# Kernel tuning notes

Hardware: AMD Instinct MI355X
Metric: run time of the kernel (lower is better)

Reference implementation:

```python
import jax, jax.numpy as jnp
import numpy as np

B, D, E, C = 16384, 2048, 16, 64  # batch, feat_dim, num_experts, classes per expert
CLASS_STARTS = np.arange(E, dtype=np.int32) * C  # contiguous equal-size class ranges


def setup_inputs() -> dict:
    key = jax.random.key(0)
    k1, k2, k3, k4, k5 = jax.random.split(key, 5)
    return {
        "features": jax.random.normal(k1, (B, D), dtype=jnp.float32),
        "coarse_w": jax.random.normal(k2, (E, D), dtype=jnp.float32) * 0.02,
        "coarse_b": jax.random.normal(k3, (E,), dtype=jnp.float32) * 0.02,
        "expert_w": jax.random.normal(k4, (E, C, D), dtype=jnp.float32) * 0.02,
        "expert_b": jax.random.normal(k5, (E, C), dtype=jnp.float32) * 0.02,
    }


def reference(features, coarse_w, coarse_b, expert_w, expert_b):
    # coarse router: Linear(feat_dim -> num_experts)
    coarse_output = features @ coarse_w.T + coarse_b          # [B, E]
    expert_id = jnp.argmax(coarse_output, axis=1)             # [B] top-1 routing

    # all-expert heads as one batched GEMM, then select routed expert per sample
    # (same math as gather-by-mask + per-expert Linear + scatter-back loop)
    y_all = jnp.einsum('bd,ecd->bec', features, expert_w) + expert_b  # [B, E, C]
    y = jnp.take_along_axis(y_all, expert_id[:, None, None], axis=1)[:, 0, :]  # [B, C]

    # local_preds: softmax probs of the routed expert (all experts have C = max classes)
    local_preds = jax.nn.softmax(y, axis=1)                   # [B, C]

    # global prediction = local argmax + expert's class-range start
    starts = jnp.asarray(CLASS_STARTS)
    global_preds = (jnp.argmax(y, axis=1) + starts[expert_id]).astype(jnp.float32)  # [B]

    return coarse_output, expert_id, local_preds, global_preds
```

## Files before the change

### kernel.cpp

```cpp
#include <hip/hip_runtime.h>
#include <cstdint>

static constexpr int B_ = 16384;
static constexpr int D_ = 2048;
static constexpr int E_ = 16;
static constexpr int C_ = 64;
static constexpr int KCH = 32;
static constexpr int TR_E = 64;
static constexpr int SK_E = 4;
static constexpr int TR_C = 128;
static constexpr int SK_C = 8;
static constexpr int MAXITEMS = (B_ / TR_E) + E_;

template <int RPT, int CPT, int NC, int TR, int SK, bool FLAT>
__global__ __launch_bounds__(256) void gemm_tile(
    const float* __restrict__ feat, const float* __restrict__ Wall,
    const int* __restrict__ rowList, const int* __restrict__ cnt,
    const int* __restrict__ sched, const int* __restrict__ nItems,
    float* __restrict__ part0,
    float* __restrict__ partRest)
{
  constexpr int FITER = TR / 32;
  constexpr int WSLOTS = NC * 8;
  constexpr int WITER = (WSLOTS + 255) / 256;
  constexpr int CG = NC / CPT;

  __shared__ float fT[KCH * TR];
  __shared__ float wT[KCH * NC];
  __shared__ int rIdx[TR];

  const int tid = threadIdx.x;
  int e, tile, kz;
  if (FLAT) {
    const int b = blockIdx.x;
    kz = b % SK;
    const int item = b / SK;
    if (item >= *nItems) return;
    const int s = sched[item];
    e = s & 255;
    tile = s >> 8;
  } else {
    e = 0;
    tile = blockIdx.x;
    kz = blockIdx.z;
  }
  const int count = cnt ? cnt[e] : B_;

  if (tid < TR) {
    const int slot = tile * TR + tid;
    rIdx[tid] = (slot < count) ? (rowList ? rowList[e * B_ + slot] : slot) : 0;
  }
  __syncthreads();

  unsigned grows[FITER];
  int dcf[FITER], sbf[FITER];
#pragma unroll
  for (int i = 0; i < FITER; ++i) {
    const int idx = i * 256 + tid;
    const int rl = idx >> 3;
    dcf[i] = idx & 7;
    grows[i] = (unsigned)rIdx[rl];
    sbf[i] = (((rl >> 3) ^ dcf[i]) << 3) + (rl & 7);
  }
  int wc[WITER], wdc[WITER], wsb[WITER];
  bool wact[WITER];
#pragma unroll
  for (int i = 0; i < WITER; ++i) {
    const int idx = i * 256 + tid;
    wact[i] = idx < WSLOTS;
    const int c = (idx < WSLOTS) ? (idx >> 3) : 0;
    wc[i] = c;
    wdc[i] = idx & 7;
    wsb[i] = (((c >> 3) ^ (wdc[i] & (NC / 8 - 1))) << 3) + (c & 7);
  }

  const int cg = tid % CG;
  const int rg = tid / CG;

  float acc[RPT][CPT];
#pragma unroll
  for (int r = 0; r < RPT; ++r)
#pragma unroll
    for (int c = 0; c < CPT; ++c) acc[r][c] = 0.f;

  const float* We = Wall + (size_t)e * NC * D_;
  constexpr int KRANGE = D_ / SK;
  constexpr int NCH = KRANGE / KCH;
  const int k0 = kz * KRANGE;

  float4 pf[FITER], pw[WITER];
#pragma unroll
  for (int i = 0; i < FITER; ++i)
    pf[i] = *(const float4*)(feat + (size_t)grows[i] * D_ + k0 + dcf[i] * 4);
#pragma unroll
  for (int i = 0; i < WITER; ++i)
    if (wact[i])
      pw[i] = *(const float4*)(We + (size_t)wc[i] * D_ + k0 + wdc[i] * 4);

  for (int ch = 0; ch < NCH; ++ch) {
#pragma unroll
    for (int i = 0; i < FITER; ++i) {
      float* p = &fT[(dcf[i] * 4) * TR + sbf[i]];
      p[0 * TR] = pf[i].x;
      p[1 * TR] = pf[i].y;
      p[2 * TR] = pf[i].z;
      p[3 * TR] = pf[i].w;
    }
#pragma unroll
    for (int i = 0; i < WITER; ++i)
      if (wact[i]) {
        float* p = &wT[(wdc[i] * 4) * NC + wsb[i]];
        p[0 * NC] = pw[i].x;
        p[1 * NC] = pw[i].y;
        p[2 * NC] = pw[i].z;
        p[3 * NC] = pw[i].w;
      }
    __syncthreads();
    if (ch + 1 < NCH) {
      const int kb = k0 + (ch + 1) * KCH;
#pragma unroll
      for (int i = 0; i < FITER; ++i)
        pf[i] = *(const float4*)(feat + (size_t)grows[i] * D_ + kb + dcf[i] * 4);
#pragma unroll
      for (int i = 0; i < WITER; ++i)
        if (wact[i])
          pw[i] = *(const float4*)(We + (size_t)wc[i] * D_ + kb + wdc[i] * 4);
    }
#pragma unroll
    for (int dd = 0; dd < KCH; ++dd) {
      const int s = dd >> 2;
      const int sw = s & (NC / 8 - 1);
      float a[RPT], bb[CPT];
#pragma unroll
      for (int r4 = 0; r4 < RPT / 4; ++r4) {
        const int col = rg * RPT + r4 * 4;
        const float4 v =
            *(const float4*)&fT[dd * TR + (((col >> 3) ^ s) << 3) + (col & 7)];
        a[r4 * 4 + 0] = v.x;
        a[r4 * 4 + 1] = v.y;
        a[r4 * 4 + 2] = v.z;
        a[r4 * 4 + 3] = v.w;
      }
      if constexpr (CPT >= 4) {
#pragma unroll
        for (int c4 = 0; c4 < CPT / 4; ++c4) {
          const int col = cg * CPT + c4 * 4;
          const float4 v =
              *(const float4*)&wT[dd * NC + (((col >> 3) ^ sw) << 3) + (col & 7)];
          bb[c4 * 4 + 0] = v.x;
          bb[c4 * 4 + 1] = v.y;
          bb[c4 * 4 + 2] = v.z;
          bb[c4 * 4 + 3] = v.w;
        }
      } else {
        const int col = cg * 2;
        const float2 v =
            *(const float2*)&wT[dd * NC + (((col >> 3) ^ sw) << 3) + (col & 7)];
        bb[0] = v.x;
        bb[1] = v.y;
      }
#pragma unroll
      for (int r = 0; r < RPT; ++r)
#pragma unroll
        for (int c = 0; c < CPT; ++c) acc[r][c] += a[r] * bb[c];
    }
    __syncthreads();
  }

  float* pk = kz ? (partRest + (size_t)(kz - 1) * B_ * NC) : part0;
#pragma unroll
  for (int r = 0; r < RPT; ++r) {
    const int lrow = rg * RPT + r;
    const int slot = tile * TR + lrow;
    if (slot < count) {
      const int grow = rIdx[lrow];
      float* dst = pk + (size_t)grow * NC + cg * CPT;
      if constexpr (CPT >= 4) {
#pragma unroll
        for (int c4 = 0; c4 < CPT / 4; ++c4)
          *(float4*)(dst + c4 * 4) =
              make_float4(acc[r][c4 * 4 + 0], acc[r][c4 * 4 + 1],
                          acc[r][c4 * 4 + 2], acc[r][c4 * 4 + 3]);
      } else {
        *(float2*)dst = make_float2(acc[r][0], acc[r][1]);
      }
    }
  }
}

__global__ __launch_bounds__(256) void coarse_finish(
    const float* __restrict__ cpart0, const float* __restrict__ cpartRest,
    const float* __restrict__ cb, float* __restrict__ out0,
    float* __restrict__ out1, int* __restrict__ eidArr, int* __restrict__ cnt,
    int* __restrict__ rowList) {
  __shared__ int lcnt[E_];
  __shared__ int lbase[E_];
  const int tid = threadIdx.x;
  if (tid < E_) lcnt[tid] = 0;
  __syncthreads();
  const int row = blockIdx.x * 256 + tid;

  float v[E_];
#pragma unroll
  for (int j = 0; j < E_; ++j) v[j] = cb[j];
#pragma unroll
  for (int kz = 0; kz < SK_C; ++kz) {
    const float* p = (kz == 0) ? (cpart0 + (size_t)row * E_)
                               : (cpartRest + ((size_t)(kz - 1) * B_ + row) * E_);
#pragma unroll
    for (int j4 = 0; j4 < E_ / 4; ++j4) {
      const float4 t = *(const float4*)(p + j4 * 4);
      v[j4 * 4 + 0] += t.x;
      v[j4 * 4 + 1] += t.y;
      v[j4 * 4 + 2] += t.z;
      v[j4 * 4 + 3] += t.w;
    }
  }
  int best = 0;
  float bv = v[0];
#pragma unroll
  for (int j = 1; j < E_; ++j)
    if (v[j] > bv) { bv = v[j]; best = j; }

  float* o0 = out0 + (size_t)row * E_;
#pragma unroll
  for (int j4 = 0; j4 < E_ / 4; ++j4)
    *(float4*)(o0 + j4 * 4) = make_float4(v[j4 * 4 + 0], v[j4 * 4 + 1],
                                          v[j4 * 4 + 2], v[j4 * 4 + 3]);
  out1[row] = (float)best;
  eidArr[row] = best;

  const int lpos = atomicAdd(&lcnt[best], 1);
  __syncthreads();
  if (tid < E_) lbase[tid] = atomicAdd(&cnt[tid], lcnt[tid]);
  __syncthreads();
  rowList[best * B_ + lbase[best] + lpos] = row;
}

__global__ void make_schedule(const int* __restrict__ cnt,
                              int* __restrict__ sched,
                              int* __restrict__ nItems) {
  __shared__ int tiles[E_];
  __shared__ int offs[E_];
  const int t = threadIdx.x;
  if (t < E_) tiles[t] = (cnt[t] + TR_E - 1) / TR_E;
  __syncthreads();
  if (t == 0) {
    int acc = 0;
    for (int e = 0; e < E_; ++e) {
      offs[e] = acc;
      acc += tiles[e];
    }
    *nItems = acc;
  }
  __syncthreads();
  if (t < E_) {
    const int o = offs[t], n = tiles[t];
    for (int k = 0; k < n; ++k) sched[o + k] = t | (k << 8);
  }
}

__global__ __launch_bounds__(256) void finish_rows(
    const float* __restrict__ ypart0, const float* __restrict__ ypartRest,
    const float* __restrict__ eb, const int* __restrict__ eidArr,
    float* __restrict__ out2, float* __restrict__ out3) {
  const int lane = threadIdx.x & 63;
  const int row = (blockIdx.x * 256 + threadIdx.x) >> 6;
  const int eid = eidArr[row];

  float v = eb[eid * C_ + lane];
  v += ypart0[(size_t)row * C_ + lane];
#pragma unroll
  for (int kz = 1; kz < SK_E; ++kz)
    v += ypartRest[((size_t)(kz - 1) * B_ + row) * C_ + lane];

  float m = v;
#pragma unroll
  for (int off = 32; off; off >>= 1) m = fmaxf(m, __shfl_xor(m, off, 64));
  const float p = __expf(v - m);
  float s = p;
#pragma unroll
  for (int off = 32; off; off >>= 1) s += __shfl_xor(s, off, 64);
  out2[(size_t)row * C_ + lane] = p / s;

  float av = v;
  int ai = lane;
#pragma unroll
  for (int off = 32; off; off >>= 1) {
    const float ov = __shfl_xor(av, off, 64);
    const int oi = __shfl_xor(ai, off, 64);
    if (ov > av || (ov == av && oi < ai)) { av = ov; ai = oi; }
  }
  if (lane == 0) out3[row] = (float)(ai + (eid << 6));
}

extern "C" void kernel_launch(void* const* d_in, const int* in_sizes, int n_in,
                              void* d_out, int out_size, void* d_ws,
                              size_t ws_size, hipStream_t stream) {
  const float* feat = (const float*)d_in[0];
  const float* cw = (const float*)d_in[1];
  const float* cb = (const float*)d_in[2];
  const float* ew = (const float*)d_in[3];
  const float* eb = (const float*)d_in[4];

  float* out0 = (float*)d_out;
  float* out1 = out0 + (size_t)B_ * E_;
  float* out2 = out1 + B_;
  float* out3 = out2 + (size_t)B_ * C_;

  char* ws = (char*)d_ws;
  float* cpartRest = (float*)ws;
  float* ypartRest = cpartRest + (size_t)(SK_C - 1) * B_ * E_;
  int* rowList = (int*)(ypartRest + (size_t)(SK_E - 1) * B_ * C_);
  int* cnt = rowList + (size_t)E_ * B_;
  int* eidArr = cnt + 64;
  int* sched = eidArr + B_;
  int* nItems = sched + 512;

  hipMemsetAsync(cnt, 0, E_ * sizeof(int), stream);

  gemm_tile<4, 2, E_, TR_C, SK_C, false>
      <<<dim3(B_ / TR_C, 1, SK_C), 256, 0, stream>>>(
          feat, cw, nullptr, nullptr, nullptr, nullptr, out0, cpartRest);
  coarse_finish<<<B_ / 256, 256, 0, stream>>>(out0, cpartRest, cb, out0, out1,
                                              eidArr, cnt, rowList);
  make_schedule<<<1, 64, 0, stream>>>(cnt, sched, nItems);
  gemm_tile<4, 4, C_, TR_E, SK_E, true>
      <<<MAXITEMS * SK_E, 256, 0, stream>>>(feat, ew, rowList, cnt, sched,
                                            nItems, out2, ypartRest);
  finish_rows<<<(B_ * 64) / 256, 256, 0, stream>>>(out2, ypartRest, eb, eidArr,
                                                   out2, out3);
}
```

Before: 298.5 us.

## Pre-transpose weights, read weights from global via scalar loads, widen tiles

Adds a kernel that transposes the expert and coarse weights into a D-major layout, then redesigns the GEMM tile. Each wave now owns a slice of columns and reads its weights straight from global memory with wave-uniform addresses, while only the features are staged in padded shared memory, and the math uses packed two-wide FMAs. Tile rows are doubled, and split-K depth is doubled when the workspace is large enough. The goals are to remove the LDS traffic and swizzle work for weights and to add parallelism. The costs are an extra transpose pass over about 8 MB of weights on every call and more partial-sum traffic in the finish kernels.

```diff
diff --git a/kernel.cpp b/kernel.cpp
--- a/kernel.cpp
+++ b/kernel.cpp
@@ -1,32 +1,70 @@
 #include <hip/hip_runtime.h>
 #include <cstdint>
+
+typedef float v2f __attribute__((ext_vector_type(2)));
 
 static constexpr int B_ = 16384;
 static constexpr int D_ = 2048;
 static constexpr int E_ = 16;
 static constexpr int C_ = 64;
 static constexpr int KCH = 32;
-static constexpr int TR_E = 64;
-static constexpr int SK_E = 4;
-static constexpr int TR_C = 128;
-static constexpr int SK_C = 8;
+
+static constexpr int TR_E = 128;
+static constexpr int TR_C = 256;
+static constexpr int SK_E_HI = 8;
+static constexpr int SK_C_HI = 16;
+static constexpr int SK_E_LO = 4;
+static constexpr int SK_C_LO = 8;
 static constexpr int MAXITEMS = (B_ / TR_E) + E_;
 
-template <int RPT, int CPT, int NC, int TR, int SK, bool FLAT>
+__global__ __launch_bounds__(256) void transpose_w(
+    const float* __restrict__ ew, const float* __restrict__ cw,
+    float* __restrict__ ewT, float* __restrict__ cwT) {
+  const int bid = blockIdx.x;
+  const int tid = threadIdx.x;
+  if (bid < 128) {
+    const int g = bid * 256 + tid;
+    const int eidx = g >> 11;
+    const int d = g & (D_ - 1);
+    const float* src = ew + ((size_t)eidx * C_) * D_ + d;
+    float* dst = ewT + ((size_t)eidx * D_ + d) * C_;
+#pragma unroll
+    for (int cc = 0; cc < C_; cc += 16) {
+      float t[16];
+#pragma unroll
+      for (int c = 0; c < 16; ++c) t[c] = src[(size_t)(cc + c) * D_];
+#pragma unroll
+      for (int q = 0; q < 4; ++q)
+        *(float4*)(dst + cc + q * 4) =
+            make_float4(t[q * 4 + 0], t[q * 4 + 1], t[q * 4 + 2], t[q * 4 + 3]);
+    }
+  } else {
+    const int d = (bid - 128) * 256 + tid;
+    float t[E_];
+#pragma unroll
+    for (int e2 = 0; e2 < E_; ++e2) t[e2] = cw[(size_t)e2 * D_ + d];
+    float* dst = cwT + (size_t)d * E_;
+#pragma unroll
+    for (int q = 0; q < 4; ++q)
+      *(float4*)(dst + q * 4) =
+          make_float4(t[q * 4 + 0], t[q * 4 + 1], t[q * 4 + 2], t[q * 4 + 3]);
+  }
+}
+
+template <int RPT, int CW, int NC, int TR, int SK, bool FLAT>
 __global__ __launch_bounds__(256) void gemm_tile(
-    const float* __restrict__ feat, const float* __restrict__ Wall,
+    const float* __restrict__ feat, const float* __restrict__ Wt,
     const int* __restrict__ rowList, const int* __restrict__ cnt,
     const int* __restrict__ sched, const int* __restrict__ nItems,
     float* __restrict__ part0,
     float* __restrict__ partRest)
 {
+  constexpr int TRP = TR + 1;
   constexpr int FITER = TR / 32;
-  constexpr int WSLOTS = NC * 8;
-  constexpr int WITER = (WSLOTS + 255) / 256;
-  constexpr int CG = NC / CPT;
-
-  __shared__ float fT[KCH * TR];
-  __shared__ float wT[KCH * NC];
+  static_assert(64 * RPT == TR, "lanes*RPT must cover tile rows");
+  static_assert(4 * CW == NC, "4 waves * CW must cover tile cols");
+
+  __shared__ float fT[KCH * TRP];
   __shared__ int rIdx[TR];
 
   const int tid = threadIdx.x;
@@ -44,6 +82,9 @@
     tile = blockIdx.x;
     kz = blockIdx.z;
   }
+  e = __builtin_amdgcn_readfirstlane(e);
+  tile = __builtin_amdgcn_readfirstlane(tile);
+  kz = __builtin_amdgcn_readfirstlane(kz);
   const int count = cnt ? cnt[e] : B_;
 
   if (tid < TR) {
@@ -53,116 +94,67 @@
   __syncthreads();
 
   unsigned grows[FITER];
-  int dcf[FITER], sbf[FITER];
+  int dcf[FITER], rls[FITER];
 #pragma unroll
   for (int i = 0; i < FITER; ++i) {
     const int idx = i * 256 + tid;
-    const int rl = idx >> 3;
+    rls[i] = idx >> 3;
     dcf[i] = idx & 7;
-    grows[i] = (unsigned)rIdx[rl];
-    sbf[i] = (((rl >> 3) ^ dcf[i]) << 3) + (rl & 7);
-  }
-  int wc[WITER], wdc[WITER], wsb[WITER];
-  bool wact[WITER];
-#pragma unroll
-  for (int i = 0; i < WITER; ++i) {
-    const int idx = i * 256 + tid;
-    wact[i] = idx < WSLOTS;
-    const int c = (idx < WSLOTS) ? (idx >> 3) : 0;
-    wc[i] = c;
-    wdc[i] = idx & 7;
-    wsb[i] = (((c >> 3) ^ (wdc[i] & (NC / 8 - 1))) << 3) + (c & 7);
-  }
-
-  const int cg = tid % CG;
-  const int rg = tid / CG;
-
-  float acc[RPT][CPT];
+    grows[i] = (unsigned)rIdx[rls[i]];
+  }
+
+  const int lane = tid & 63;
+  const int w = __builtin_amdgcn_readfirstlane(tid >> 6);
+  const int wcol = w * CW;
+
+  v2f acc[RPT][CW / 2];
 #pragma unroll
   for (int r = 0; r < RPT; ++r)
 #pragma unroll
-    for (int c = 0; c < CPT; ++c) acc[r][c] = 0.f;
-
-  const float* We = Wall + (size_t)e * NC * D_;
+    for (int j = 0; j < CW / 2; ++j) acc[r][j] = (v2f){0.f, 0.f};
+
   constexpr int KRANGE = D_ / SK;
   constexpr int NCH = KRANGE / KCH;
   const int k0 = kz * KRANGE;
-
-  float4 pf[FITER], pw[WITER];
+  const float* Wb = Wt + (size_t)e * D_ * NC;
+
+  float4 pf[FITER];
 #pragma unroll
   for (int i = 0; i < FITER; ++i)
     pf[i] = *(const float4*)(feat + (size_t)grows[i] * D_ + k0 + dcf[i] * 4);
-#pragma unroll
-  for (int i = 0; i < WITER; ++i)
-    if (wact[i])
-      pw[i] = *(const float4*)(We + (size_t)wc[i] * D_ + k0 + wdc[i] * 4);
 
   for (int ch = 0; ch < NCH; ++ch) {
 #pragma unroll
     for (int i = 0; i < FITER; ++i) {
-      float* p = &fT[(dcf[i] * 4) * TR + sbf[i]];
-      p[0 * TR] = pf[i].x;
-      p[1 * TR] = pf[i].y;
-      p[2 * TR] = pf[i].z;
-      p[3 * TR] = pf[i].w;
-    }
-#pragma unroll
-    for (int i = 0; i < WITER; ++i)
-      if (wact[i]) {
-        float* p = &wT[(wdc[i] * 4) * NC + wsb[i]];
-        p[0 * NC] = pw[i].x;
-        p[1 * NC] = pw[i].y;
-        p[2 * NC] = pw[i].z;
-        p[3 * NC] = pw[i].w;
-      }
+      float* p = &fT[(dcf[i] * 4) * TRP + rls[i]];
+      p[0 * TRP] = pf[i].x;
+      p[1 * TRP] = pf[i].y;
+      p[2 * TRP] = pf[i].z;
+      p[3 * TRP] = pf[i].w;
+    }
     __syncthreads();
     if (ch + 1 < NCH) {
       const int kb = k0 + (ch + 1) * KCH;
 #pragma unroll
       for (int i = 0; i < FITER; ++i)
         pf[i] = *(const float4*)(feat + (size_t)grows[i] * D_ + kb + dcf[i] * 4);
-#pragma unroll
-      for (int i = 0; i < WITER; ++i)
-        if (wact[i])
-          pw[i] = *(const float4*)(We + (size_t)wc[i] * D_ + kb + wdc[i] * 4);
-    }
+    }
+    const float* wrow = Wb + (size_t)(k0 + ch * KCH) * NC + wcol;
 #pragma unroll
     for (int dd = 0; dd < KCH; ++dd) {
-      const int s = dd >> 2;
-      const int sw = s & (NC / 8 - 1);
-      float a[RPT], bb[CPT];
-#pragma unroll
-      for (int r4 = 0; r4 < RPT / 4; ++r4) {
-        const int col = rg * RPT + r4 * 4;
-        const float4 v =
-            *(const float4*)&fT[dd * TR + (((col >> 3) ^ s) << 3) + (col & 7)];
-        a[r4 * 4 + 0] = v.x;
-        a[r4 * 4 + 1] = v.y;
-        a[r4 * 4 + 2] = v.z;
-        a[r4 * 4 + 3] = v.w;
+      v2f b2[CW / 2];
+      const v2f* wp = (const v2f*)(wrow + (size_t)dd * NC);
+#pragma unroll
+      for (int j = 0; j < CW / 2; ++j) b2[j] = wp[j];
+      float a[RPT];
+#pragma unroll
+      for (int r = 0; r < RPT; ++r) a[r] = fT[dd * TRP + lane + 64 * r];
+#pragma unroll
+      for (int r = 0; r < RPT; ++r) {
+        const v2f ar = {a[r], a[r]};
+#pragma unroll
+        for (int j = 0; j < CW / 2; ++j) acc[r][j] += ar * b2[j];
       }
-      if constexpr (CPT >= 4) {
-#pragma unroll
-        for (int c4 = 0; c4 < CPT / 4; ++c4) {
-          const int col = cg * CPT + c4 * 4;
-          const float4 v =
-              *(const float4*)&wT[dd * NC + (((col >> 3) ^ sw) << 3) + (col & 7)];
-          bb[c4 * 4 + 0] = v.x;
-          bb[c4 * 4 + 1] = v.y;
-          bb[c4 * 4 + 2] = v.z;
-          bb[c4 * 4 + 3] = v.w;
-        }
-      } else {
-        const int col = cg * 2;
-        const float2 v =
-            *(const float2*)&wT[dd * NC + (((col >> 3) ^ sw) << 3) + (col & 7)];
-        bb[0] = v.x;
-        bb[1] = v.y;
-      }
-#pragma unroll
-      for (int r = 0; r < RPT; ++r)
-#pragma unroll
-        for (int c = 0; c < CPT; ++c) acc[r][c] += a[r] * bb[c];
     }
     __syncthreads();
   }
@@ -170,24 +162,21 @@
   float* pk = kz ? (partRest + (size_t)(kz - 1) * B_ * NC) : part0;
 #pragma unroll
   for (int r = 0; r < RPT; ++r) {
-    const int lrow = rg * RPT + r;
+    const int lrow = lane + 64 * r;
     const int slot = tile * TR + lrow;
     if (slot < count) {
       const int grow = rIdx[lrow];
-      float* dst = pk + (size_t)grow * NC + cg * CPT;
-      if constexpr (CPT >= 4) {
-#pragma unroll
-        for (int c4 = 0; c4 < CPT / 4; ++c4)
-          *(float4*)(dst + c4 * 4) =
-              make_float4(acc[r][c4 * 4 + 0], acc[r][c4 * 4 + 1],
-                          acc[r][c4 * 4 + 2], acc[r][c4 * 4 + 3]);
-      } else {
-        *(float2*)dst = make_float2(acc[r][0], acc[r][1]);
-      }
-    }
-  }
-}
-
+      float* dst = pk + (size_t)grow * NC + wcol;
+#pragma unroll
+      for (int j4 = 0; j4 < CW / 4; ++j4)
+        *(float4*)(dst + j4 * 4) =
+            make_float4(acc[r][j4 * 2][0], acc[r][j4 * 2][1],
+                        acc[r][j4 * 2 + 1][0], acc[r][j4 * 2 + 1][1]);
+    }
+  }
+}
+
+template <int SK>
 __global__ __launch_bounds__(256) void coarse_finish(
     const float* __restrict__ cpart0, const float* __restrict__ cpartRest,
     const float* __restrict__ cb, float* __restrict__ out0,
@@ -204,7 +193,7 @@
 #pragma unroll
   for (int j = 0; j < E_; ++j) v[j] = cb[j];
 #pragma unroll
-  for (int kz = 0; kz < SK_C; ++kz) {
+  for (int kz = 0; kz < SK; ++kz) {
     const float* p = (kz == 0) ? (cpart0 + (size_t)row * E_)
                                : (cpartRest + ((size_t)(kz - 1) * B_ + row) * E_);
 #pragma unroll
@@ -260,6 +249,7 @@
   }
 }
 
+template <int SK>
 __global__ __launch_bounds__(256) void finish_rows(
     const float* __restrict__ ypart0, const float* __restrict__ ypartRest,
     const float* __restrict__ eb, const int* __restrict__ eidArr,
@@ -271,7 +261,7 @@
   float v = eb[eid * C_ + lane];
   v += ypart0[(size_t)row * C_ + lane];
 #pragma unroll
-  for (int kz = 1; kz < SK_E; ++kz)
+  for (int kz = 1; kz < SK; ++kz)
     v += ypartRest[((size_t)(kz - 1) * B_ + row) * C_ + lane];
 
   float m = v;
@@ -308,26 +298,48 @@
   float* out2 = out1 + B_;
   float* out3 = out2 + (size_t)B_ * C_;
 
-  char* ws = (char*)d_ws;
-  float* cpartRest = (float*)ws;
-  float* ypartRest = cpartRest + (size_t)(SK_C - 1) * B_ * E_;
-  int* rowList = (int*)(ypartRest + (size_t)(SK_E - 1) * B_ * C_);
-  int* cnt = rowList + (size_t)E_ * B_;
-  int* eidArr = cnt + 64;
-  int* sched = eidArr + B_;
-  int* nItems = sched + 512;
+  const bool HI = ws_size >= (size_t)56 * 1024 * 1024;
+  const int skC = HI ? SK_C_HI : SK_C_LO;
+  const int skE = HI ? SK_E_HI : SK_E_LO;
+
+  char* p = (char*)d_ws;
+  float* cwT = (float*)p;            p += (size_t)D_ * E_ * 4;
+  float* ewT = (float*)p;            p += (size_t)E_ * D_ * C_ * 4;
+  float* cpartRest = (float*)p;      p += (size_t)(skC - 1) * B_ * E_ * 4;
+  float* ypartRest = (float*)p;      p += (size_t)(skE - 1) * B_ * C_ * 4;
+  int* rowList = (int*)p;            p += (size_t)E_ * B_ * 4;
+  int* cnt = (int*)p;                p += 64 * 4;
+  int* eidArr = (int*)p;             p += (size_t)B_ * 4;
+  int* sched = (int*)p;              p += 512 * 4;
+  int* nItems = (int*)p;
 
   hipMemsetAsync(cnt, 0, E_ * sizeof(int), stream);
 
-  gemm_tile<4, 2, E_, TR_C, SK_C, false>
-      <<<dim3(B_ / TR_C, 1, SK_C), 256, 0, stream>>>(
-          feat, cw, nullptr, nullptr, nullptr, nullptr, out0, cpartRest);
-  coarse_finish<<<B_ / 256, 256, 0, stream>>>(out0, cpartRest, cb, out0, out1,
-                                              eidArr, cnt, rowList);
-  make_schedule<<<1, 64, 0, stream>>>(cnt, sched, nItems);
-  gemm_tile<4, 4, C_, TR_E, SK_E, true>
-      <<<MAXITEMS * SK_E, 256, 0, stream>>>(feat, ew, rowList, cnt, sched,
-                                            nItems, out2, ypartRest);
-  finish_rows<<<(B_ * 64) / 256, 256, 0, stream>>>(out2, ypartRest, eb, eidArr,
-                                                   out2, out3);
-}
+  transpose_w<<<136, 256, 0, stream>>>(ew, cw, ewT, cwT);
+
+  if (HI) {
+    gemm_tile<4, 4, E_, TR_C, SK_C_HI, false>
+        <<<dim3(B_ / TR_C, 1, SK_C_HI), 256, 0, stream>>>(
+            feat, cwT, nullptr, nullptr, nullptr, nullptr, out0, cpartRest);
+    coarse_finish<SK_C_HI><<<B_ / 256, 256, 0, stream>>>(
+        out0, cpartRest, cb, out0, out1, eidArr, cnt, rowList);
+    make_schedule<<<1, 64, 0, stream>>>(cnt, sched, nItems);
+    gemm_tile<2, 16, C_, TR_E, SK_E_HI, true>
+        <<<MAXITEMS * SK_E_HI, 256, 0, stream>>>(feat, ewT, rowList, cnt,
+                                                 sched, nItems, out2, ypartRest);
+    finish_rows<SK_E_HI><<<(B_ * 64) / 256, 256, 0, stream>>>(
+        out2, ypartRest, eb, eidArr, out2, out3);
+  } else {
+    gemm_tile<4, 4, E_, TR_C, SK_C_LO, false>
+        <<<dim3(B_ / TR_C, 1, SK_C_LO), 256, 0, stream>>>(
+            feat, cwT, nullptr, nullptr, nullptr, nullptr, out0, cpartRest);
+    coarse_finish<SK_C_LO><<<B_ / 256, 256, 0, stream>>>(
+        out0, cpartRest, cb, out0, out1, eidArr, cnt, rowList);
+    make_schedule<<<1, 64, 0, stream>>>(cnt, sched, nItems);
+    gemm_tile<2, 16, C_, TR_E, SK_E_LO, true>
+        <<<MAXITEMS * SK_E_LO, 256, 0, stream>>>(feat, ewT, rowList, cnt,
+                                                 sched, nItems, out2, ypartRest);
+    finish_rows<SK_E_LO><<<(B_ * 64) / 256, 256, 0, stream>>>(
+        out2, ypartRest, eb, eidArr, out2, out3);
+  }
+}
```

New measurement: 349.2 us. +17.0%, slower.
